# Performance work log

Hardware: AMD Instinct MI355X
Metric: run time of the kernel (lower is better)

Reference implementation:

```python
import jax, jax.numpy as jnp
import numpy as np

LN_EPS = 1e-5

def _layer_norm(x, g, b):
    mu = jnp.mean(x, axis=-1, keepdims=True)
    var = jnp.mean(jnp.square(x - mu), axis=-1, keepdims=True)
    return (x - mu) * jax.lax.rsqrt(var + LN_EPS) * g + b

def _conv(x, src, tgt, N, alphas, ws, W3, W_self, bias, deg_power):
    # alphas, ws: tuples of 3 per-edge [E] arrays (sp, ctx, lat)
    # W3: [3, in, out]; deg_power: [3]
    out = x @ W_self + bias  # self loop + bias, [N, out]
    for c in range(3):
        eff = alphas[c] * ws[c]                                   # [E]
        deg = jnp.ones((N,), x.dtype).at[tgt].add(eff)            # [N]
        dinv = jnp.power(jnp.clip(deg, 1e-6), deg_power[c])       # [N]
        norm = eff * dinv[tgt] * dinv[src]                        # [E]
        h = x @ W3[c]                                             # [N, out] (linear => transform before gather)
        msg = norm[:, None] * h[src]                              # [E, out]
        out = out + jax.ops.segment_sum(msg, tgt, num_segments=N)
    return out

def setup_inputs() -> dict:
    N, E, D, L = 50000, 1000000, 128, 2
    key = jax.random.key(0)
    ks = jax.random.split(key, 16)
    scale = 1.0 / np.sqrt(D)
    inp = {
        "x": jax.random.normal(ks[0], (N, D), jnp.float32),
        "edge_index": jax.random.randint(ks[1], (2, E), 0, N, jnp.int32),
        "alpha_sp": jax.random.uniform(ks[2], (E,), jnp.float32),
        "alpha_ctx": jax.random.uniform(ks[3], (E,), jnp.float32),
        "alpha_lat": jax.random.uniform(ks[4], (E,), jnp.float32),
        "w_sp": jax.random.uniform(ks[5], (E,), jnp.float32),
        "w_ctx": jax.random.uniform(ks[6], (E,), jnp.float32),
        "w_lat": jax.random.uniform(ks[7], (E,), jnp.float32),
        # stacked per-layer params: [L, 3, in, out] for the three channel weights
        "W3": jax.random.normal(ks[8], (L, 3, D, D), jnp.float32) * scale,
        "W_self": jax.random.normal(ks[9], (L, D, D), jnp.float32) * scale,
        "bias": jnp.zeros((L, D), jnp.float32),
        "deg_power": jnp.full((L, 3), -0.5, jnp.float32),
        "ln_g": jnp.ones((D,), jnp.float32),
        "ln_b": jnp.zeros((D,), jnp.float32),
        "num_nodes": N,
    }
    return inp

def reference(x, edge_index, alpha_sp, alpha_ctx, alpha_lat, w_sp, w_ctx, w_lat,
              W3, W_self, bias, deg_power, ln_g, ln_b, num_nodes):
    N = num_nodes
    src, tgt = edge_index[0], edge_index[1]
    alphas = (alpha_sp, alpha_ctx, alpha_lat)
    ws = (w_sp, w_ctx, w_lat)
    L = W3.shape[0]
    h = x
    for i in range(L):
        h = _conv(h, src, tgt, N, alphas, ws, W3[i], W_self[i], bias[i], deg_power[i])
        if i < L - 1:
            h = _layer_norm(h, ln_g, ln_b)
            h = jax.nn.relu(h)
            # dropout: eval mode (identity)
    return h
```

## Files before the change

### kernel.cpp

```cpp
#include <hip/hip_runtime.h>
#include <hip/hip_bf16.h>

typedef short bf16x8 __attribute__((ext_vector_type(8)));
typedef float f32x4 __attribute__((ext_vector_type(4)));

#define BSH 7
#define BK  (1 << BSH)

static inline int cdiv(int a, int b){ return (a + b - 1) / b; }

__device__ __forceinline__ unsigned pack_bf16_hi(float v){
    return ((unsigned)__bfloat16_as_ushort(__float2bfloat16(v))) << 16;
}
__device__ __forceinline__ float bf16hi_to_f32(unsigned bits_hi16){
    return __uint_as_float(bits_hi16);
}

__global__ __launch_bounds__(256) void k_bcnt0(const int* __restrict__ tgt,
                                               int* __restrict__ gcnt, int E, int NB){
    __shared__ int lh[1024];
    int tid = threadIdx.x;
    for (int b = tid; b < 1024; b += 256) lh[b] = 0;
    __syncthreads();
    int c0 = blockIdx.x * 4096;
    #pragma unroll
    for (int u = 0; u < 16; ++u){
        int e = c0 + u * 256 + tid;
        if (e < E) atomicAdd(&lh[tgt[e] >> BSH], 1);
    }
    __syncthreads();
    for (int b = tid; b < NB; b += 256){
        int c = lh[b];
        if (c) atomicAdd(&gcnt[b], c);
    }
}

__global__ __launch_bounds__(256) void k_bscan(const int* __restrict__ gcnt,
                                               int* __restrict__ bbase,
                                               int* __restrict__ gcur,
                                               int* __restrict__ rs,
                                               int N, int E){
    __shared__ int sc[256];
    int tid = threadIdx.x;
    int b0 = tid * 4;
    int v0 = gcnt[b0], v1 = gcnt[b0 + 1], v2 = gcnt[b0 + 2], v3 = gcnt[b0 + 3];
    int t3 = v0 + v1 + v2 + v3;
    sc[tid] = t3;
    __syncthreads();
    for (int off = 1; off < 256; off <<= 1){
        int x = (tid >= off) ? sc[tid - off] : 0;
        __syncthreads();
        sc[tid] += x;
        __syncthreads();
    }
    int ex = sc[tid] - t3;
    bbase[b0]     = ex;
    bbase[b0 + 1] = ex + v0;
    bbase[b0 + 2] = ex + v0 + v1;
    bbase[b0 + 3] = ex + v0 + v1 + v2;
    gcur[b0] = bbase[b0]; gcur[b0 + 1] = bbase[b0 + 1];
    gcur[b0 + 2] = bbase[b0 + 2]; gcur[b0 + 3] = bbase[b0 + 3];
    if (tid == 255) bbase[1024] = sc[255];
    if (tid == 0)   rs[N] = E;
}

__global__ __launch_bounds__(256) void k_bin(
        const int* __restrict__ src, const int* __restrict__ tgt,
        const float* __restrict__ asp, const float* __restrict__ actx,
        const float* __restrict__ alat, const float* __restrict__ wsp,
        const float* __restrict__ wctx, const float* __restrict__ wlat,
        int* __restrict__ gcur, uint4* __restrict__ binned, int E, int NB){
    __shared__ int lh[1024], lo[1024], lc[1024], gb[1024], tsum[256];
    __shared__ unsigned sx[4096], sy[4096];
    __shared__ int st[4096];
    int tid = threadIdx.x;
    int c0 = blockIdx.x * 4096;
    int cnt = E - c0; if (cnt > 4096) cnt = 4096;
    for (int b = tid; b < 1024; b += 256){ lh[b] = 0; lc[b] = 0; }
    __syncthreads();
    #pragma unroll
    for (int u = 0; u < 16; ++u){
        int e = c0 + u * 256 + tid;
        if (e < E) atomicAdd(&lh[tgt[e] >> BSH], 1);
    }
    __syncthreads();
    int b4 = tid * 4;
    int v0 = lh[b4], v1 = lh[b4 + 1], v2 = lh[b4 + 2], v3 = lh[b4 + 3];
    int t3 = v0 + v1 + v2 + v3;
    tsum[tid] = t3;
    __syncthreads();
    for (int off = 1; off < 256; off <<= 1){
        int x = (tid >= off) ? tsum[tid - off] : 0;
        __syncthreads();
        tsum[tid] += x;
        __syncthreads();
    }
    int ex = tsum[tid] - t3;
    lo[b4] = ex; lo[b4 + 1] = ex + v0; lo[b4 + 2] = ex + v0 + v1; lo[b4 + 3] = ex + v0 + v1 + v2;
    for (int b = tid; b < NB; b += 256){
        int c = lh[b];
        gb[b] = c ? atomicAdd(&gcur[b], c) : 0;
    }
    __syncthreads();
    #pragma unroll
    for (int u = 0; u < 16; ++u){
        int e = c0 + u * 256 + tid;
        if (e < E){
            int t = tgt[e];
            int b = t >> BSH;
            int p = lo[b] + atomicAdd(&lc[b], 1);
            sx[p] = (unsigned)src[e] | pack_bf16_hi(asp[e] * wsp[e]);
            sy[p] = (pack_bf16_hi(actx[e] * wctx[e]) >> 16) | pack_bf16_hi(alat[e] * wlat[e]);
            st[p] = t;
        }
    }
    __syncthreads();
    for (int i = tid; i < cnt; i += 256){
        int t = st[i];
        int b = t >> BSH;
        int g = gb[b] + (i - lo[b]);
        uint4 o = {sx[i], sy[i], (unsigned)t, 0u};
        binned[g] = o;
    }
}

__global__ __launch_bounds__(256) void k_bucket(
        const uint4* __restrict__ binned, const int* __restrict__ bbase,
        uint2* __restrict__ effo, int* __restrict__ rs, int N){
    __shared__ int th[128], sc2[128], cur[128];
    int tid = threadIdx.x;
    int b = blockIdx.x;
    int t0 = b << BSH;
    int ebeg = bbase[b], eend = bbase[b + 1];
    if (tid < 128) th[tid] = 0;
    __syncthreads();
    for (int i = ebeg + tid; i < eend; i += 256)
        atomicAdd(&th[(int)binned[i].z - t0], 1);
    __syncthreads();
    int v = (tid < 128) ? th[tid] : 0;
    if (tid < 128) sc2[tid] = v;
    __syncthreads();
    for (int off = 1; off < 128; off <<= 1){
        int x = (tid >= off && tid < 128) ? sc2[tid - off] : 0;
        __syncthreads();
        if (tid < 128) sc2[tid] += x;
        __syncthreads();
    }
    if (tid < 128){
        int exv = sc2[tid] - v;
        cur[tid] = exv;
        int t = t0 + tid;
        if (t < N) rs[t] = ebeg + exv;
    }
    __syncthreads();
    for (int i = ebeg + tid; i < eend; i += 256){
        uint4 r = binned[i];
        int loc = (int)r.z - t0;
        int p = atomicAdd(&cur[loc], 1);
        uint2 o = {r.x, r.y};
        effo[ebeg + p] = o;
    }
}

__global__ __launch_bounds__(256) void k_deg(
        const uint2* __restrict__ effo, const int* __restrict__ rs,
        const float* __restrict__ dp,
        float* __restrict__ dinv_all,
        int N, int L){
    int n = blockIdx.x * 256 + threadIdx.x;
    if (n >= N) return;
    int beg = rs[n], end = rs[n + 1];
    float s0 = 0.f, s1 = 0.f, s2 = 0.f;
    for (int i = beg; i < end; ++i){
        uint2 v = effo[i];
        s0 += bf16hi_to_f32(v.x & 0xFFFF0000u);
        s1 += bf16hi_to_f32(v.y << 16);
        s2 += bf16hi_to_f32(v.y & 0xFFFF0000u);
    }
    float d0 = fmaxf(1.f + s0, 1e-6f);
    float d1 = fmaxf(1.f + s1, 1e-6f);
    float d2 = fmaxf(1.f + s2, 1e-6f);
    for (int l = 0; l < L; ++l){
        size_t base = ((size_t)l * N + n) * 3;
        dinv_all[base + 0] = powf(d0, dp[l * 3 + 0]);
        dinv_all[base + 1] = powf(d1, dp[l * 3 + 1]);
        dinv_all[base + 2] = powf(d2, dp[l * 3 + 2]);
    }
}

__global__ void k_normv(const uint2* __restrict__ effo,
                        const float* __restrict__ dinv_all,
                        uint2* __restrict__ nv, int E, int N, int L){
    int i = blockIdx.x * 256 + threadIdx.x;
    if (i >= L * E) return;
    int l = i / E;
    int e = i - l * E;
    const float* dinv = dinv_all + (size_t)l * N * 3;
    uint2 v = effo[e];
    unsigned s = v.x & 0xFFFFu;
    float e0 = bf16hi_to_f32(v.x & 0xFFFF0000u);
    float e1 = bf16hi_to_f32(v.y << 16);
    float e2 = bf16hi_to_f32(v.y & 0xFFFF0000u);
    float n0 = e0 * dinv[3 * s + 0];
    float n1 = e1 * dinv[3 * s + 1];
    float n2 = e2 * dinv[3 * s + 2];
    uint2 o;
    o.x = s | pack_bf16_hi(n0);
    o.y = (pack_bf16_hi(n1) >> 16) | pack_bf16_hi(n2);
    nv[i] = o;
}

__global__ void k_x2bf(const float* __restrict__ x, __hip_bfloat16* __restrict__ Ap, int n){
    int i = blockIdx.x * 256 + threadIdx.x;
    if (i < n) Ap[(size_t)(i >> 7) * 512 + (i & 127)] = __float2bfloat16(x[i]);
}

__global__ void k_wcat(const float* __restrict__ Wself,
                       const float* __restrict__ W3,
                       __hip_bfloat16* __restrict__ BT,
                       int L){
    int i = blockIdx.x * 256 + threadIdx.x;
    if (i >= L * 65536) return;
    int l = i >> 16, r = i & 65535;
    int j = r >> 9, k = r & 511;
    float v;
    if (k < 128) v = Wself[l * 16384 + k * 128 + j];
    else {
        int c = (k >> 7) - 1, kk = k & 127;
        v = W3[l * 49152 + (c * 128 + kk) * 128 + j];
    }
    BT[i] = __float2bfloat16(v);
}

__global__ __launch_bounds__(256) void k_msg(
        __hip_bfloat16* __restrict__ Ap,
        const uint2* __restrict__ nv,
        const int* __restrict__ rs,
        const float* __restrict__ dinv,
        int N){
    int w = threadIdx.x >> 6, lane = threadIdx.x & 63;
    int t = blockIdx.x * 4 + w;
    if (t >= N) return;
    float ax0 = 0.f, ay0 = 0.f, ax1 = 0.f, ay1 = 0.f, ax2 = 0.f, ay2 = 0.f;
    int beg = rs[t], end = rs[t + 1];
    int i = beg;
    for (; i + 16 <= end; i += 16){
        uint2 m[16];
        #pragma unroll
        for (int u = 0; u < 16; ++u) m[u] = nv[i + u];
        float2 f[16];
        #pragma unroll
        for (int u = 0; u < 16; ++u){
            const __hip_bfloat162* p =
                (const __hip_bfloat162*)(Ap + (size_t)(m[u].x & 0xFFFFu) * 512);
            f[u] = __bfloat1622float2(p[lane]);
        }
        #pragma unroll
        for (int u = 0; u < 16; ++u){
            float n0 = bf16hi_to_f32(m[u].x & 0xFFFF0000u);
            float n1 = bf16hi_to_f32(m[u].y << 16);
            float n2 = bf16hi_to_f32(m[u].y & 0xFFFF0000u);
            ax0 += n0 * f[u].x; ay0 += n0 * f[u].y;
            ax1 += n1 * f[u].x; ay1 += n1 * f[u].y;
            ax2 += n2 * f[u].x; ay2 += n2 * f[u].y;
        }
    }
    for (; i + 4 <= end; i += 4){
        uint2 m[4];
        #pragma unroll
        for (int u = 0; u < 4; ++u) m[u] = nv[i + u];
        float2 f[4];
        #pragma unroll
        for (int u = 0; u < 4; ++u){
            const __hip_bfloat162* p =
                (const __hip_bfloat162*)(Ap + (size_t)(m[u].x & 0xFFFFu) * 512);
            f[u] = __bfloat1622float2(p[lane]);
        }
        #pragma unroll
        for (int u = 0; u < 4; ++u){
            float n0 = bf16hi_to_f32(m[u].x & 0xFFFF0000u);
            float n1 = bf16hi_to_f32(m[u].y << 16);
            float n2 = bf16hi_to_f32(m[u].y & 0xFFFF0000u);
            ax0 += n0 * f[u].x; ay0 += n0 * f[u].y;
            ax1 += n1 * f[u].x; ay1 += n1 * f[u].y;
            ax2 += n2 * f[u].x; ay2 += n2 * f[u].y;
        }
    }
    for (; i < end; ++i){
        uint2 m = nv[i];
        const __hip_bfloat162* p =
            (const __hip_bfloat162*)(Ap + (size_t)(m.x & 0xFFFFu) * 512);
        float2 fv = __bfloat1622float2(p[lane]);
        float n0 = bf16hi_to_f32(m.x & 0xFFFF0000u);
        float n1 = bf16hi_to_f32(m.y << 16);
        float n2 = bf16hi_to_f32(m.y & 0xFFFF0000u);
        ax0 += n0 * fv.x; ay0 += n0 * fv.y;
        ax1 += n1 * fv.x; ay1 += n1 * fv.y;
        ax2 += n2 * fv.x; ay2 += n2 * fv.y;
    }
    float dt0 = dinv[3 * t], dt1 = dinv[3 * t + 1], dt2 = dinv[3 * t + 2];
    __hip_bfloat162* yo = (__hip_bfloat162*)(Ap + (size_t)t * 512 + 128) + lane;
    float2 r0 = {dt0 * ax0, dt0 * ay0};
    float2 r1 = {dt1 * ax1, dt1 * ay1};
    float2 r2 = {dt2 * ax2, dt2 * ay2};
    yo[0]   = __float22bfloat162_rn(r0);
    yo[64]  = __float22bfloat162_rn(r1);
    yo[128] = __float22bfloat162_rn(r2);
}

__global__ __launch_bounds__(256) void k_gemm(
        const __hip_bfloat16* __restrict__ A,
        const __hip_bfloat16* __restrict__ BT,
        const float* __restrict__ bias,
        float* __restrict__ outbuf,
        int M, int doLN,
        const float* __restrict__ g, const float* __restrict__ b,
        __hip_bfloat16* __restrict__ Ap){
    __shared__ __hip_bfloat16 As[128 * 128];
    __shared__ __hip_bfloat16 Bs[128 * 128];
    const int tid = threadIdx.x;
    const int row0 = blockIdx.x * 128;
    const int w = tid >> 6, lane = tid & 63;
    const int wm = (w & 1) * 64, wn = (w >> 1) * 64;
    const int lm = lane & 15, lq = lane >> 4;

    f32x4 acc[4][4];
    #pragma unroll
    for (int mt = 0; mt < 4; ++mt)
        #pragma unroll
        for (int nt = 0; nt < 4; ++nt)
            acc[mt][nt] = {0.f, 0.f, 0.f, 0.f};

    for (int kt = 0; kt < 4; ++kt){
        #pragma unroll
        for (int it = 0; it < 8; ++it){
            int v = it * 256 + tid;
            int r = v >> 4, c = v & 15;
            int soff = r * 128 + ((c ^ (r & 15)) << 3);
            int4 av = {0, 0, 0, 0};
            if (row0 + r < M)
                av = *(const int4*)(A + (size_t)(row0 + r) * 512 + kt * 128 + (c << 3));
            *(int4*)(&As[soff]) = av;
            int4 bv = *(const int4*)(BT + (size_t)r * 512 + kt * 128 + (c << 3));
            *(int4*)(&Bs[soff]) = bv;
        }
        __syncthreads();

        #pragma unroll
        for (int kk = 0; kk < 4; ++kk){
            int kc = kk * 4 + lq;
            bf16x8 a[4], b2[4];
            #pragma unroll
            for (int mt = 0; mt < 4; ++mt){
                int r = wm + mt * 16 + lm;
                a[mt] = *(const bf16x8*)(&As[r * 128 + ((kc ^ (r & 15)) << 3)]);
            }
            #pragma unroll
            for (int nt = 0; nt < 4; ++nt){
                int r = wn + nt * 16 + lm;
                b2[nt] = *(const bf16x8*)(&Bs[r * 128 + ((kc ^ (r & 15)) << 3)]);
            }
            #pragma unroll
            for (int mt = 0; mt < 4; ++mt)
                #pragma unroll
                for (int nt = 0; nt < 4; ++nt)
                    acc[mt][nt] = __builtin_amdgcn_mfma_f32_16x16x32_bf16(
                        a[mt], b2[nt], acc[mt][nt], 0, 0, 0);
        }
        __syncthreads();
    }

    if (!doLN){
        #pragma unroll
        for (int mt = 0; mt < 4; ++mt){
            #pragma unroll
            for (int nt = 0; nt < 4; ++nt){
                int col = wn + nt * 16 + lm;
                #pragma unroll
                for (int r = 0; r < 4; ++r){
                    int row = row0 + wm + mt * 16 + lq * 4 + r;
                    if (row < M)
                        outbuf[(size_t)row * 128 + col] = acc[mt][nt][r] + bias[col];
                }
            }
        }
    } else {
        float* S1 = (float*)As;
        float* S2 = S1 + 4096;
        float* MS = (float*)Bs;
        const int half = wn >> 6;
        const int slot = half * 16 + lm;
        float bv[4];
        #pragma unroll
        for (int nt = 0; nt < 4; ++nt) bv[nt] = bias[wn + nt * 16 + lm];
        #pragma unroll
        for (int mt = 0; mt < 4; ++mt){
            #pragma unroll
            for (int r = 0; r < 4; ++r){
                int rl = wm + mt * 16 + lq * 4 + r;
                float ps = 0.f, pq = 0.f;
                #pragma unroll
                for (int nt = 0; nt < 4; ++nt){
                    float v = acc[mt][nt][r] + bv[nt];
                    ps += v; pq += v * v;
                }
                S1[rl * 32 + slot] = ps;
                S2[rl * 32 + slot] = pq;
            }
        }
        __syncthreads();
        if (tid < 128){
            float s = 0.f, sq = 0.f;
            #pragma unroll
            for (int j = 0; j < 32; ++j){
                s  += S1[tid * 32 + j];
                sq += S2[tid * 32 + j];
            }
            float mu = s * (1.0f / 128.0f);
            float var = sq * (1.0f / 128.0f) - mu * mu;
            MS[tid] = mu;
            MS[128 + tid] = rsqrtf(var + 1e-5f);
        }
        __syncthreads();
        float gv[4], bbv[4];
        #pragma unroll
        for (int nt = 0; nt < 4; ++nt){
            int col = wn + nt * 16 + lm;
            gv[nt] = g[col]; bbv[nt] = b[col];
        }
        #pragma unroll
        for (int mt = 0; mt < 4; ++mt){
            #pragma unroll
            for (int r = 0; r < 4; ++r){
                int rl = wm + mt * 16 + lq * 4 + r;
                int row = row0 + rl;
                if (row < M){
                    float mu = MS[rl], sc = MS[128 + rl];
                    #pragma unroll
                    for (int nt = 0; nt < 4; ++nt){
                        int col = wn + nt * 16 + lm;
                        float v = acc[mt][nt][r] + bv[nt];
                        float y = fmaxf((v - mu) * sc * gv[nt] + bbv[nt], 0.0f);
                        Ap[(size_t)row * 512 + col] = __float2bfloat16(y);
                    }
                }
            }
        }
    }
}

extern "C" void kernel_launch(void* const* d_in, const int* in_sizes, int n_in,
                              void* d_out, int out_size, void* d_ws, size_t ws_size,
                              hipStream_t stream) {
    const float* x     = (const float*)d_in[0];
    const int*   ei    = (const int*)d_in[1];
    const float* asp   = (const float*)d_in[2];
    const float* actx  = (const float*)d_in[3];
    const float* alat  = (const float*)d_in[4];
    const float* wsp   = (const float*)d_in[5];
    const float* wctx  = (const float*)d_in[6];
    const float* wlat  = (const float*)d_in[7];
    const float* W3    = (const float*)d_in[8];
    const float* Wself = (const float*)d_in[9];
    const float* bias  = (const float*)d_in[10];
    const float* dpow  = (const float*)d_in[11];
    const float* lng   = (const float*)d_in[12];
    const float* lnb   = (const float*)d_in[13];

    const int N = in_sizes[0] / 128;
    const int E = in_sizes[1] / 2;
    const int L = in_sizes[8] / (3 * 128 * 128);
    const int NB = cdiv(N, BK);
    const int* src = ei;
    const int* tgt = ei + E;

    char* p = (char*)d_ws;
    auto alloc = [&](size_t bytes) -> void* {
        void* r = (void*)p;
        p += (bytes + 255) & ~(size_t)255;
        return r;
    };
    int*   rs       = (int*)  alloc((size_t)(N + 1) * 4);
    int*   gcnt     = (int*)  alloc(1024 * 4);
    int*   bbase    = (int*)  alloc(1025 * 4);
    int*   gcur     = (int*)  alloc(1024 * 4);
    uint2* effo     = (uint2*)alloc((size_t)E * 8);
    uint2* nv       = (uint2*)alloc((size_t)L * E * 8);
    float* dinv_all = (float*)alloc((size_t)L * N * 3 * 4);
    __hip_bfloat16* Ap = (__hip_bfloat16*)alloc((size_t)N * 512 * 2);
    __hip_bfloat16* BT = (__hip_bfloat16*)alloc((size_t)L * 128 * 512 * 2);
    uint4* binned = (uint4*)nv;

    hipMemsetAsync(gcnt, 0, 1024 * 4, stream);
    k_bcnt0 <<<cdiv(E, 4096), 256, 0, stream>>>(tgt, gcnt, E, NB);
    k_bscan <<<1, 256, 0, stream>>>(gcnt, bbase, gcur, rs, N, E);
    k_bin   <<<cdiv(E, 4096), 256, 0, stream>>>(src, tgt, asp, actx, alat, wsp, wctx, wlat,
                                                gcur, binned, E, NB);
    k_bucket<<<NB, 256, 0, stream>>>(binned, bbase, effo, rs, N);
    k_deg   <<<cdiv(N, 256), 256, 0, stream>>>(effo, rs, dpow, dinv_all, N, L);
    k_x2bf  <<<cdiv(N * 128, 256), 256, 0, stream>>>(x, Ap, N * 128);
    k_wcat  <<<cdiv(L * 65536, 256), 256, 0, stream>>>(Wself, W3, BT, L);
    k_normv <<<cdiv(L * E, 256), 256, 0, stream>>>(effo, dinv_all, nv, E, N, L);

    for (int l = 0; l < L; ++l){
        int doLN = (l < L - 1) ? 1 : 0;
        const float* dinv_l = dinv_all + (size_t)l * N * 3;
        k_msg <<<cdiv(N, 4), 256, 0, stream>>>(Ap, nv + (size_t)l * E, rs, dinv_l, N);
        k_gemm<<<cdiv(N, 128), 256, 0, stream>>>(Ap, BT + (size_t)l * 65536,
                                                 bias + l * 128, (float*)d_out, N,
                                                 doLN, lng, lnb, Ap);
    }
}
```

Measured before the change: 363.8 us.

## Scatter binned edges directly to global and shrink message unroll to 8

The binning kernel drops its shared-memory staging, local prefix scan and second coalescing pass. Each edge is now written straight to its global bucket slot via a per-bucket atomic offset, which removes several barriers and about 48KB of LDS per block but makes the global writes scattered. The message kernel replaces its 16-wide and 4-wide unrolled gather loops with a single 8-wide loop, which lowers register pressure at the cost of fewer loads in flight.

```diff
diff --git a/kernel.cpp b/kernel.cpp
--- a/kernel.cpp
+++ b/kernel.cpp
@@ -70,12 +70,9 @@
         const float* __restrict__ alat, const float* __restrict__ wsp,
         const float* __restrict__ wctx, const float* __restrict__ wlat,
         int* __restrict__ gcur, uint4* __restrict__ binned, int E, int NB){
-    __shared__ int lh[1024], lo[1024], lc[1024], gb[1024], tsum[256];
-    __shared__ unsigned sx[4096], sy[4096];
-    __shared__ int st[4096];
+    __shared__ int lh[1024], lc[1024], gb[1024];
     int tid = threadIdx.x;
     int c0 = blockIdx.x * 4096;
-    int cnt = E - c0; if (cnt > 4096) cnt = 4096;
     for (int b = tid; b < 1024; b += 256){ lh[b] = 0; lc[b] = 0; }
     __syncthreads();
     #pragma unroll
@@ -84,19 +81,6 @@
         if (e < E) atomicAdd(&lh[tgt[e] >> BSH], 1);
     }
     __syncthreads();
-    int b4 = tid * 4;
-    int v0 = lh[b4], v1 = lh[b4 + 1], v2 = lh[b4 + 2], v3 = lh[b4 + 3];
-    int t3 = v0 + v1 + v2 + v3;
-    tsum[tid] = t3;
-    __syncthreads();
-    for (int off = 1; off < 256; off <<= 1){
-        int x = (tid >= off) ? tsum[tid - off] : 0;
-        __syncthreads();
-        tsum[tid] += x;
-        __syncthreads();
-    }
-    int ex = tsum[tid] - t3;
-    lo[b4] = ex; lo[b4 + 1] = ex + v0; lo[b4 + 2] = ex + v0 + v1; lo[b4 + 3] = ex + v0 + v1 + v2;
     for (int b = tid; b < NB; b += 256){
         int c = lh[b];
         gb[b] = c ? atomicAdd(&gcur[b], c) : 0;
@@ -108,19 +92,14 @@
         if (e < E){
             int t = tgt[e];
             int b = t >> BSH;
-            int p = lo[b] + atomicAdd(&lc[b], 1);
-            sx[p] = (unsigned)src[e] | pack_bf16_hi(asp[e] * wsp[e]);
-            sy[p] = (pack_bf16_hi(actx[e] * wctx[e]) >> 16) | pack_bf16_hi(alat[e] * wlat[e]);
-            st[p] = t;
-        }
-    }
-    __syncthreads();
-    for (int i = tid; i < cnt; i += 256){
-        int t = st[i];
-        int b = t >> BSH;
-        int g = gb[b] + (i - lo[b]);
-        uint4 o = {sx[i], sy[i], (unsigned)t, 0u};
-        binned[g] = o;
+            int p = gb[b] + atomicAdd(&lc[b], 1);
+            uint4 o;
+            o.x = (unsigned)src[e] | pack_bf16_hi(asp[e] * wsp[e]);
+            o.y = (pack_bf16_hi(actx[e] * wctx[e]) >> 16) | pack_bf16_hi(alat[e] * wlat[e]);
+            o.z = (unsigned)t;
+            o.w = 0u;
+            binned[p] = o;
+        }
     }
 }
 
@@ -244,40 +223,19 @@
     float ax0 = 0.f, ay0 = 0.f, ax1 = 0.f, ay1 = 0.f, ax2 = 0.f, ay2 = 0.f;
     int beg = rs[t], end = rs[t + 1];
     int i = beg;
-    for (; i + 16 <= end; i += 16){
-        uint2 m[16];
-        #pragma unroll
-        for (int u = 0; u < 16; ++u) m[u] = nv[i + u];
-        float2 f[16];
-        #pragma unroll
-        for (int u = 0; u < 16; ++u){
+    for (; i + 8 <= end; i += 8){
+        uint2 m[8];
+        #pragma unroll
+        for (int u = 0; u < 8; ++u) m[u] = nv[i + u];
+        float2 f[8];
+        #pragma unroll
+        for (int u = 0; u < 8; ++u){
             const __hip_bfloat162* p =
                 (const __hip_bfloat162*)(Ap + (size_t)(m[u].x & 0xFFFFu) * 512);
             f[u] = __bfloat1622float2(p[lane]);
         }
         #pragma unroll
-        for (int u = 0; u < 16; ++u){
-            float n0 = bf16hi_to_f32(m[u].x & 0xFFFF0000u);
-            float n1 = bf16hi_to_f32(m[u].y << 16);
-            float n2 = bf16hi_to_f32(m[u].y & 0xFFFF0000u);
-            ax0 += n0 * f[u].x; ay0 += n0 * f[u].y;
-            ax1 += n1 * f[u].x; ay1 += n1 * f[u].y;
-            ax2 += n2 * f[u].x; ay2 += n2 * f[u].y;
-        }
-    }
-    for (; i + 4 <= end; i += 4){
-        uint2 m[4];
-        #pragma unroll
-        for (int u = 0; u < 4; ++u) m[u] = nv[i + u];
-        float2 f[4];
-        #pragma unroll
-        for (int u = 0; u < 4; ++u){
-            const __hip_bfloat162* p =
-                (const __hip_bfloat162*)(Ap + (size_t)(m[u].x & 0xFFFFu) * 512);
-            f[u] = __bfloat1622float2(p[lane]);
-        }
-        #pragma unroll
-        for (int u = 0; u < 4; ++u){
+        for (int u = 0; u < 8; ++u){
             float n0 = bf16hi_to_f32(m[u].x & 0xFFFF0000u);
             float n1 = bf16hi_to_f32(m[u].y << 16);
             float n2 = bf16hi_to_f32(m[u].y & 0xFFFF0000u);
```

Result: faster. 349.4 us (-4.0%).
